# Performance work log

Measured on AMD Instinct MI355X. Metric: run time of the kernel, lower is better.

Reference implementation:

```python
import jax, jax.numpy as jnp
import numpy as np

B, S, IN, OUT = 4, 2048, 4096, 4096


def setup_inputs() -> dict:
    key = jax.random.key(0)
    k_x, k_w, k_s, k_b = jax.random.split(key, 4)
    x = jax.random.normal(k_x, (B, S, IN), dtype=jnp.float16)
    # int8 quantized weight, layout [in_features, out_features] (torch.t(weight) in __init__)
    w_q = jax.random.randint(k_w, (IN, OUT), -128, 128, dtype=jnp.int32).astype(jnp.int8)
    # per-output-channel dequant scale (typical w8 per-channel scale magnitude)
    scale = (jax.random.uniform(k_s, (OUT,), dtype=jnp.float32) * 0.02 + 0.001).astype(jnp.float16)
    bias = jax.random.normal(k_b, (OUT,), dtype=jnp.float16)
    return {"x": x, "w_q": w_q, "scale": scale, "bias": bias}


def reference(x, w_q, scale, bias):
    # w8_a16_gemm: inline dequant int8 -> fp16 via per-column scale, then GEMM in fp16
    w = w_q.astype(jnp.float16) * scale[None, :]          # [in, out]
    out = jnp.einsum('bsi,io->bso', x, w)                 # [B, S, out]
    return out + bias
```

## Files before the change

kernel.cpp:

```cpp
#include <hip/hip_runtime.h>
#include <stdint.h>


typedef __attribute__((ext_vector_type(4))) float     f32x4;
typedef __attribute__((ext_vector_type(8))) _Float16  f16x8;

#define M_DIM 8192
#define N_DIM 4096
#define K_DIM 4096

__global__ __launch_bounds__(256) void convert_x_to_f16(const float* __restrict__ x,
                                                        _Float16* __restrict__ Xh) {
    const size_t i = ((size_t)blockIdx.x * 256 + threadIdx.x) * 8;
    float4 v0 = *(const float4*)(x + i);
    float4 v1 = *(const float4*)(x + i + 4);
    f16x8 h;
    h[0] = (_Float16)v0.x; h[1] = (_Float16)v0.y; h[2] = (_Float16)v0.z; h[3] = (_Float16)v0.w;
    h[4] = (_Float16)v1.x; h[5] = (_Float16)v1.y; h[6] = (_Float16)v1.z; h[7] = (_Float16)v1.w;
    *(f16x8*)(Xh + i) = h;
}

__global__ __launch_bounds__(256) void dequant_w_to_f16(const int* __restrict__ wq,
                                                        _Float16* __restrict__ Wt) {
    __shared__ _Float16 tile[64][65];
    const int n0 = blockIdx.x * 64;
    const int k0 = blockIdx.y * 64;
    const int t  = threadIdx.x;
    const int r  = t >> 2;
    const int c0 = (t & 3) * 16;
    const int* src = wq + (size_t)(k0 + r) * N_DIM + n0 + c0;
#pragma unroll
    for (int j = 0; j < 4; ++j) {
        int4 q = *(const int4*)(src + j * 4);
        tile[c0 + j * 4 + 0][r] = (_Float16)q.x;
        tile[c0 + j * 4 + 1][r] = (_Float16)q.y;
        tile[c0 + j * 4 + 2][r] = (_Float16)q.z;
        tile[c0 + j * 4 + 3][r] = (_Float16)q.w;
    }
    __syncthreads();
    const int nn  = t >> 2;
    const int cc0 = (t & 3) * 16;
    _Float16 vals[16] __attribute__((aligned(16)));
#pragma unroll
    for (int j = 0; j < 16; ++j) vals[j] = tile[nn][cc0 + j];
    _Float16* dst = Wt + (size_t)(n0 + nn) * K_DIM + k0 + cc0;
    *(float4*)(dst + 0) = *(const float4*)(vals + 0);
    *(float4*)(dst + 8) = *(const float4*)(vals + 8);
}

#define AS1C(p) (const __attribute__((address_space(1))) void*)(p)
#define AS3C(p) (__attribute__((address_space(3))) void*)(p)

#define STAGE_TILE(BB, tl) do {                                                       \
    __builtin_amdgcn_global_load_lds(AS1C(aStageBase + (size_t)(tl) * 32),            \
        AS3C(ldsBase + (BB) + t * 16), 16, 0, 0);                                     \
    __builtin_amdgcn_global_load_lds(AS1C(aStageBase + aHalfJump + (size_t)(tl) * 32),\
        AS3C(ldsBase + (BB) + 8192 + t * 16), 16, 0, 0);                              \
    __builtin_amdgcn_global_load_lds(AS1C(bStageBase + (size_t)(tl) * 32),            \
        AS3C(ldsBase + (BB) + 16384 + t * 16), 16, 0, 0);                             \
    __builtin_amdgcn_global_load_lds(AS1C(bStageBase + bHalfJump + (size_t)(tl) * 32),\
        AS3C(ldsBase + (BB) + 24576 + t * 16), 16, 0, 0);                             \
} while (0)

#define DSR(dst, addr, IMM) \
    asm volatile("ds_read_b128 %0, %1 offset:%c2" : "=v"(dst) : "v"(addr), "i"(IMM))

#define READS(AR, BR, IB)                                    \
    DSR(a0, AR, (IB) + 0 * 1024);                            \
    DSR(a1, AR, (IB) + 1 * 1024);                            \
    DSR(a2, AR, (IB) + 2 * 1024);                            \
    DSR(a3, AR, (IB) + 3 * 1024);                            \
    DSR(a4, AR, (IB) + 4 * 1024);                            \
    DSR(a5, AR, (IB) + 5 * 1024);                            \
    DSR(a6, AR, (IB) + 6 * 1024);                            \
    DSR(a7, AR, (IB) + 7 * 1024);                            \
    DSR(b0, BR, (IB) + 16384 + 0 * 1024);                    \
    DSR(b1, BR, (IB) + 16384 + 1 * 1024);                    \
    DSR(b2, BR, (IB) + 16384 + 2 * 1024);                    \
    DSR(b3, BR, (IB) + 16384 + 3 * 1024)

#define MM(AI, NI, AV, BV) \
    acc[AI][NI] = __builtin_amdgcn_mfma_f32_16x16x32_f16(AV, BV, acc[AI][NI], 0, 0, 0)

#define MFMA32()                                                          \
    MM(0, 0, a0, b0); MM(0, 1, a0, b1); MM(0, 2, a0, b2); MM(0, 3, a0, b3); \
    MM(1, 0, a1, b0); MM(1, 1, a1, b1); MM(1, 2, a1, b2); MM(1, 3, a1, b3); \
    MM(2, 0, a2, b0); MM(2, 1, a2, b1); MM(2, 2, a2, b2); MM(2, 3, a2, b3); \
    MM(3, 0, a3, b0); MM(3, 1, a3, b1); MM(3, 2, a3, b2); MM(3, 3, a3, b3); \
    MM(4, 0, a4, b0); MM(4, 1, a4, b1); MM(4, 2, a4, b2); MM(4, 3, a4, b3); \
    MM(5, 0, a5, b0); MM(5, 1, a5, b1); MM(5, 2, a5, b2); MM(5, 3, a5, b3); \
    MM(6, 0, a6, b0); MM(6, 1, a6, b1); MM(6, 2, a6, b2); MM(6, 3, a6, b3); \
    MM(7, 0, a7, b0); MM(7, 1, a7, b1); MM(7, 2, a7, b2); MM(7, 3, a7, b3)

#define BARR()  __builtin_amdgcn_s_barrier()
#define SB0()   __builtin_amdgcn_sched_barrier(0)
#define LGKM0() do { asm volatile("s_waitcnt lgkmcnt(0)" ::: "memory"); SB0(); } while (0)
#define VMC4()  asm volatile("s_waitcnt vmcnt(4)" ::: "memory")
#define PRIO1() __builtin_amdgcn_s_setprio(1)
#define PRIO0() __builtin_amdgcn_s_setprio(0)

#define INTERVAL(CRA, CRB, CIB, PRA, PRB, PIB, SBB, tl) do {                          \
    if (odd) { READS(PRA, PRB, PIB); }         \
    VMC4();                                            \
    BARR();                                                   \
    STAGE_TILE((SBB), (tl));                                                          \
    if (!odd) { READS(CRA, CRB, CIB); }                                               \
    LGKM0(); PRIO1(); MFMA32(); PRIO0();                                              \
} while (0)

__global__ __launch_bounds__(512, 2) void gemm_po(const _Float16* __restrict__ Xh,
                                                  const _Float16* __restrict__ Wt,
                                                  const float* __restrict__ scale,
                                                  const float* __restrict__ bias,
                                                  float* __restrict__ C) {
    __shared__ __attribute__((aligned(128))) _Float16 L[65536];
    char* ldsBase = (char*)L;

    const int bid = blockIdx.x;
    const int swz = (bid & 7) * 64 + (bid >> 3);
    const int bm  = swz >> 4;
    const int bn  = swz & 15;

    const int t  = threadIdx.x;
    const int l  = t & 63;
    const int w  = t >> 6;
    const int wm = (w & 3) >> 1;
    const int wn = ((w & 3) & 1) * 2 + (w >> 2);
    const int odd = __builtin_amdgcn_readfirstlane(w >> 2);

    const int lr = l & 15, lh = l >> 4;

    const int rowIdx = t >> 2;
    const int kbSw   = ((t & 3) ^ ((rowIdx >> 1) & 3)) * 16;
    const _Float16* aStageBase = Xh + (size_t)(bm * 256 + rowIdx) * K_DIM + (kbSw >> 1);
    const _Float16* bStageBase = Wt + (size_t)(bn * 256 + rowIdx) * K_DIM + (kbSw >> 1);
    const size_t aHalfJump = (size_t)128 * K_DIM;
    const size_t bHalfJump = (size_t)128 * K_DIM;

    const uint32_t xr   = (uint32_t)((lh ^ ((lr >> 1) & 3)) << 4);
    const uint32_t aoff = (uint32_t)((wm * 128 + lr) * 64) + xr;
    const uint32_t boff = (uint32_t)((wn * 64 + lr) * 64) + xr;
    const uint32_t aLo  = (uint32_t)(uintptr_t)L + aoff;
    const uint32_t aHi  = (uint32_t)(uintptr_t)L + 65536 + aoff;
    const uint32_t bLo  = (uint32_t)(uintptr_t)L + boff;
    const uint32_t bHi  = (uint32_t)(uintptr_t)L + 65536 + boff;

    f16x8 a0, a1, a2, a3, a4, a5, a6, a7, b0, b1, b2, b3;
    f32x4 acc[8][4] = {};

    {
        f16x8 z = {};
#pragma unroll
        for (int k = 0; k < 4; ++k)
            *(f16x8*)(ldsBase + 98304 + t * 64 + k * 16) = z;
    }
    __syncthreads();

    STAGE_TILE(0 * 32768, 0);
    STAGE_TILE(1 * 32768, 1);

#pragma unroll 1
    for (int it = 0; it < 32; ++it) {
        const int base = it * 4;
        const int t2 = (base + 2) & 127;
        const int t3 = (base + 3) & 127;
        const int t4 = (base + 4) & 127;
        const int t5 = (base + 5) & 127;
        INTERVAL(aLo, bLo, 0,      aHi, bHi, 32768, 2 * 32768, t2);
        INTERVAL(aLo, bLo, 32768,  aLo, bLo, 0,     3 * 32768, t3);
        INTERVAL(aHi, bHi, 0,      aLo, bLo, 32768, 0 * 32768, t4);
        INTERVAL(aHi, bHi, 32768,  aHi, bHi, 0,     1 * 32768, t5);
    }
    if (odd) {
        READS(aHi, bHi, 32768);
        LGKM0(); PRIO1(); MFMA32(); PRIO0();
    }
    asm volatile("s_waitcnt vmcnt(0)" ::: "memory");

    const int col0 = bn * 256 + wn * 64 + lr;
    const int row0 = bm * 256 + wm * 128 + lh * 4;
    float sc[4], bi[4];
#pragma unroll
    for (int ni = 0; ni < 4; ++ni) {
        sc[ni] = scale[col0 + ni * 16];
        bi[ni] = bias[col0 + ni * 16];
    }
#pragma unroll
    for (int ai = 0; ai < 8; ++ai)
#pragma unroll
        for (int r = 0; r < 4; ++r) {
            const size_t rowOff = (size_t)(row0 + ai * 16 + r) * N_DIM;
#pragma unroll
            for (int ni = 0; ni < 4; ++ni)
                C[rowOff + col0 + ni * 16] = acc[ai][ni][r] * sc[ni] + bi[ni];
        }
}

extern "C" void kernel_launch(void* const* d_in, const int* in_sizes, int n_in,
                              void* d_out, int out_size, void* d_ws, size_t ws_size,
                              hipStream_t stream) {
    const float* x     = (const float*)d_in[0];
    const int*   wq    = (const int*)d_in[1];
    const float* scale = (const float*)d_in[2];
    const float* bias  = (const float*)d_in[3];
    float* out = (float*)d_out;

    const size_t needW = (size_t)N_DIM * K_DIM * sizeof(_Float16);
    _Float16* Wt = (_Float16*)d_ws;
    _Float16* Xh = (_Float16*)((char*)d_ws + needW);

    dim3 tgrid(N_DIM / 64, K_DIM / 64);
    dequant_w_to_f16<<<tgrid, 256, 0, stream>>>(wq, Wt);
    convert_x_to_f16<<<((size_t)M_DIM * K_DIM) / (256 * 8), 256, 0, stream>>>(x, Xh);

    const int nblocks = (M_DIM / 256) * (N_DIM / 256);
    gemm_po<<<nblocks, 512, 0, stream>>>(Xh, Wt, scale, bias, out);
}
```

Measured before the change: 326.8 us.

## Replace ping-pong wave scheduling with cooperative windowed pipeline and deeper prefetch

Drops the odd/even wave ping-pong schedule, in which half the waves were offset by one phase. All waves now run a common window: compute MFMAs on registers already read, then issue LDS reads for the next subtile, stage the next global tile, wait and barrier. Three tiles are prefetched before the loop instead of two, and the wave-to-tile mapping becomes a simple 2x4 grid. The goal is to overlap LDS reads and global loads with MFMA work without staggered waves, at the cost of every wave contending for LDS and the matrix units at the same time.

After: 284.2 us. 13.0% less time.

```diff
diff --git a/kernel.cpp b/kernel.cpp
--- a/kernel.cpp
+++ b/kernel.cpp
@@ -99,16 +99,16 @@
 #define PRIO1() __builtin_amdgcn_s_setprio(1)
 #define PRIO0() __builtin_amdgcn_s_setprio(0)
 
-#define INTERVAL(CRA, CRB, CIB, PRA, PRB, PIB, SBB, tl) do {                          \
-    if (odd) { READS(PRA, PRB, PIB); }         \
-    VMC4();                                            \
-    BARR();                                                   \
-    STAGE_TILE((SBB), (tl));                                                          \
-    if (!odd) { READS(CRA, CRB, CIB); }                                               \
-    LGKM0(); PRIO1(); MFMA32(); PRIO0();                                              \
+#define WINDOW(RA, RB, RIB, SBB, tl) do {                                             \
+    LGKM0();                                     \
+    PRIO1(); MFMA32(); PRIO0();                                                       \
+    READS(RA, RB, RIB);                              \
+    STAGE_TILE((SBB), (tl));                                            \
+    VMC4();                                     \
+    BARR();                                                                           \
 } while (0)
 
-__global__ __launch_bounds__(512, 2) void gemm_po(const _Float16* __restrict__ Xh,
+__global__ __launch_bounds__(512, 2) void gemm_cw(const _Float16* __restrict__ Xh,
                                                   const _Float16* __restrict__ Wt,
                                                   const float* __restrict__ scale,
                                                   const float* __restrict__ bias,
@@ -124,10 +124,7 @@
     const int t  = threadIdx.x;
     const int l  = t & 63;
     const int w  = t >> 6;
-    const int wm = (w & 3) >> 1;
-    const int wn = ((w & 3) & 1) * 2 + (w >> 2);
-    const int odd = __builtin_amdgcn_readfirstlane(w >> 2);
-
+    const int wm = w >> 2, wn = w & 3;
     const int lr = l & 15, lh = l >> 4;
 
     const int rowIdx = t >> 2;
@@ -148,33 +145,22 @@
     f16x8 a0, a1, a2, a3, a4, a5, a6, a7, b0, b1, b2, b3;
     f32x4 acc[8][4] = {};
 
-    {
-        f16x8 z = {};
-#pragma unroll
-        for (int k = 0; k < 4; ++k)
-            *(f16x8*)(ldsBase + 98304 + t * 64 + k * 16) = z;
-    }
-    __syncthreads();
-
     STAGE_TILE(0 * 32768, 0);
     STAGE_TILE(1 * 32768, 1);
+    STAGE_TILE(2 * 32768, 2);
+    VMC4();
+    BARR();
+    READS(aLo, bLo, 0);
 
 #pragma unroll 1
     for (int it = 0; it < 32; ++it) {
         const int base = it * 4;
-        const int t2 = (base + 2) & 127;
-        const int t3 = (base + 3) & 127;
-        const int t4 = (base + 4) & 127;
-        const int t5 = (base + 5) & 127;
-        INTERVAL(aLo, bLo, 0,      aHi, bHi, 32768, 2 * 32768, t2);
-        INTERVAL(aLo, bLo, 32768,  aLo, bLo, 0,     3 * 32768, t3);
-        INTERVAL(aHi, bHi, 0,      aLo, bLo, 32768, 0 * 32768, t4);
-        INTERVAL(aHi, bHi, 32768,  aHi, bHi, 0,     1 * 32768, t5);
+        WINDOW(aLo, bLo, 32768, 3 * 32768, (base + 3) & 127);
+        WINDOW(aHi, bHi, 0,     0 * 32768, (base + 4) & 127);
+        WINDOW(aHi, bHi, 32768, 1 * 32768, (base + 5) & 127);
+        WINDOW(aLo, bLo, 0,     2 * 32768, (base + 6) & 127);
     }
-    if (odd) {
-        READS(aHi, bHi, 32768);
-        LGKM0(); PRIO1(); MFMA32(); PRIO0();
-    }
+    asm volatile("s_waitcnt lgkmcnt(0)" ::: "memory");
     asm volatile("s_waitcnt vmcnt(0)" ::: "memory");
 
     const int col0 = bn * 256 + wn * 64 + lr;
@@ -214,5 +200,5 @@
     convert_x_to_f16<<<((size_t)M_DIM * K_DIM) / (256 * 8), 256, 0, stream>>>(x, Xh);
 
     const int nblocks = (M_DIM / 256) * (N_DIM / 256);
-    gemm_po<<<nblocks, 512, 0, stream>>>(Xh, Wt, scale, bias, out);
-}
+    gemm_cw<<<nblocks, 512, 0, stream>>>(Xh, Wt, scale, bias, out);
+}
```
